# Kernel optimization log

Measured on AMD Instinct MI355X. Metric: run time of the kernel, lower is better.

The kernel has to match this reference:

```python
import jax, jax.numpy as jnp
import numpy as np

NI = 50000      # input nodes
NO = 50000      # output nodes
DEG = 16        # uniform neighborhood size -> E = NO*DEG
E = NO * DEG
FI = 64         # input feature dim
UNITS = 64
D = 3           # coord feature dim


def setup_inputs() -> dict:
    key = jax.random.key(0)
    k1, k2, k3, k4 = jax.random.split(key, 4)
    node_features = jax.random.normal(k1, (NI, FI), dtype=jnp.float32)
    coord_features = jax.random.normal(k2, (E, D), dtype=jnp.float32)
    indices = jax.random.randint(k3, (E,), 0, NI, dtype=jnp.int64)
    # uniform ragged structure: each output node has DEG edges
    row_splits = (jnp.arange(NO + 1, dtype=jnp.int64) * DEG)
    W = jax.random.normal(k4, (FI, UNITS * D), dtype=jnp.float32) * (1.0 / np.sqrt(FI))
    b = jnp.zeros((UNITS * D,), dtype=jnp.float32)
    return {"node_features": node_features, "coord_features": coord_features,
            "indices": indices, "row_splits": row_splits, "W": W, "b": b}


def reference(node_features, coord_features, indices, row_splits, W, b):
    # Dense projection on input nodes: [Ni, units*D]
    h = node_features @ W + b
    # gather_first=False path of ragged_convolution_transpose: gather after dense
    g = h[indices]                       # [E, units*D]
    g = g.reshape(-1, UNITS, D)          # [E, units, D]
    # contract over coord dim: f_eu = sum_d g_eud * coord_ed
    f = jnp.einsum('eud,ed->eu', g, coord_features)  # [E, units]
    # activation is None (identity)
    # ragged segment-sum via row_splits -> segment ids per edge
    num_out = row_splits.shape[0] - 1
    row_lengths = jnp.diff(row_splits)
    seg_ids = jnp.repeat(jnp.arange(num_out), row_lengths,
                         total_repeat_length=f.shape[0])
    out = jax.ops.segment_sum(f, seg_ids, num_segments=num_out)  # [No, units]
    return out
```

## Files before the change

### kernel.cpp

```cpp
#include <hip/hip_runtime.h>


#define NO 50000
#define DEG 16
#define FI 64
#define UNITS 64
#define KK 192
#define TN 16
#define NSTEP 6
#define GPAD 200
#define NBLK 1024
#define NTILES (NO / TN)

typedef __attribute__((ext_vector_type(8))) short short8;
typedef __attribute__((ext_vector_type(4))) float float4v;

static __device__ __forceinline__ unsigned int asu(float x){ union{float f;unsigned int u;}c; c.f=x; return c.u; }
static __device__ __forceinline__ float asf(unsigned int x){ union{unsigned int u;float f;}c; c.u=x; return c.f; }

__global__ __launch_bounds__(256, 4)
void rct3(const float* __restrict__ nf, const float* __restrict__ coord,
          const int* __restrict__ idx, const float* __restrict__ W,
          const float* __restrict__ b, float* __restrict__ out)
{
    __shared__ __align__(16) unsigned short Ghi[2][TN][GPAD];
    __shared__ __align__(16) unsigned short Glo[2][TN][GPAD];
    __shared__ float Cs[2][TN][4];

    const int tid  = threadIdx.x;
    const int w    = tid >> 6;
    const int lane = tid & 63;
    const int m16  = lane & 15;
    const int quad = lane >> 4;

    const int u = 16 * w + m16;
    short8 Bhi[NSTEP], Blo[NSTEP];
    #pragma unroll
    for (int s = 0; s < NSTEP; ++s) {
        #pragma unroll
        for (int j = 0; j < 8; ++j) {
            const int k = s * 32 + quad * 8 + j;
            const int i = k / 3, d = k - 3 * i;
            const float v = W[i * KK + 3 * u + d];
            const unsigned int vb = asu(v);
            const unsigned int rh = (vb + 0x7FFFu + ((vb >> 16) & 1u)) >> 16;
            const float hf = asf(rh << 16);
            Bhi[s][j] = (short)rh;
            Blo[s][j] = (short)(asu(v - hf) >> 16);
        }
    }
    const float b0 = b[3*u+0], b1 = b[3*u+1], b2 = b[3*u+2];

    int pp = 0;
    for (int t = blockIdx.x; t < NTILES; t += NBLK, pp ^= 1) {
        const int node0 = t * TN;

        #pragma unroll
        for (int r = 0; r < 4; ++r) {
            const int n  = 4 * w + r;
            const int eb = (node0 + n) * DEG;
            float a0=0.f,a1=0.f,a2=0.f,c0s=0.f,c1s=0.f,c2s=0.f;
            #pragma unroll
            for (int j = 0; j < DEG; ++j) {
                const int e  = __builtin_amdgcn_readfirstlane(eb + j);
                const int id = __builtin_amdgcn_readfirstlane(idx[e]);
                const float c0 = coord[3*e+0];
                const float c1 = coord[3*e+1];
                const float c2 = coord[3*e+2];
                const float v  = nf[id * FI + lane];
                a0 += v*c0; a1 += v*c1; a2 += v*c2;
                c0s += c0; c1s += c1; c2s += c2;
            }
            const unsigned int x0=asu(a0), x1=asu(a1), x2=asu(a2);
            Ghi[pp][n][3*lane+0] = (unsigned short)(x0>>16);
            Ghi[pp][n][3*lane+1] = (unsigned short)(x1>>16);
            Ghi[pp][n][3*lane+2] = (unsigned short)(x2>>16);
            Glo[pp][n][3*lane+0] = (unsigned short)(asu(a0 - asf(x0 & 0xFFFF0000u))>>16);
            Glo[pp][n][3*lane+1] = (unsigned short)(asu(a1 - asf(x1 & 0xFFFF0000u))>>16);
            Glo[pp][n][3*lane+2] = (unsigned short)(asu(a2 - asf(x2 & 0xFFFF0000u))>>16);
            if (lane == 0) {
                Cs[pp][n][0]=c0s; Cs[pp][n][1]=c1s; Cs[pp][n][2]=c2s; Cs[pp][n][3]=0.f;
            }
        }
        __syncthreads();

        float4v acc = {0.f, 0.f, 0.f, 0.f};
        #pragma unroll
        for (int s = 0; s < NSTEP; ++s) {
            const short8 Ahi = *(const short8*)(&Ghi[pp][m16][s*32 + quad*8]);
            const short8 Alo = *(const short8*)(&Glo[pp][m16][s*32 + quad*8]);
            acc = __builtin_amdgcn_mfma_f32_16x16x32_bf16(Ahi, Bhi[s], acc, 0, 0, 0);
            acc = __builtin_amdgcn_mfma_f32_16x16x32_bf16(Ahi, Blo[s], acc, 0, 0, 0);
            acc = __builtin_amdgcn_mfma_f32_16x16x32_bf16(Alo, Bhi[s], acc, 0, 0, 0);
        }

        #pragma unroll
        for (int reg = 0; reg < 4; ++reg) {
            const int row = quad * 4 + reg;
            const float4v c = *(const float4v*)(&Cs[pp][row][0]);
            out[(node0 + row) * UNITS + u] =
                acc[reg] + c[0]*b0 + c[1]*b1 + c[2]*b2;
        }
    }
}

extern "C" void kernel_launch(void* const* d_in, const int* in_sizes, int n_in,
                              void* d_out, int out_size, void* d_ws, size_t ws_size,
                              hipStream_t stream) {
    const float* nf    = (const float*)d_in[0];
    const float* coord = (const float*)d_in[1];
    const int*   idx   = (const int*)d_in[2];
    const float* W     = (const float*)d_in[4];
    const float* b     = (const float*)d_in[5];
    float* out = (float*)d_out;

    rct3<<<dim3(NBLK), dim3(256), 0, stream>>>(nf, coord, idx, W, b, out);
}
```

Before: 111.0 us.

## Prefetch edge indices and coords per-lane, broadcast via readlane, raise occupancy

Each wave now loads its 64 edge indices and coordinates in one coalesced per-lane load instead of scalar/broadcast loads per edge, then broadcasts them with readlane inside the gather loop. Metadata for the next tile is prefetched during the current tile, and the coordinate sums are computed by a shuffle reduction. The grid size and launch-bounds occupancy hint are also raised. This targets the latency of the serialized scalar index loads, at the cost of extra registers and readlane instructions.

```diff
diff --git a/kernel.cpp b/kernel.cpp
--- a/kernel.cpp
+++ b/kernel.cpp
@@ -9,7 +9,7 @@
 #define TN 16
 #define NSTEP 6
 #define GPAD 200
-#define NBLK 1024
+#define NBLK 1536
 #define NTILES (NO / TN)
 
 typedef __attribute__((ext_vector_type(8))) short short8;
@@ -17,15 +17,18 @@
 
 static __device__ __forceinline__ unsigned int asu(float x){ union{float f;unsigned int u;}c; c.f=x; return c.u; }
 static __device__ __forceinline__ float asf(unsigned int x){ union{unsigned int u;float f;}c; c.u=x; return c.f; }
+static __device__ __forceinline__ float rdlane_f(float v, int l){
+    return asf((unsigned int)__builtin_amdgcn_readlane((int)asu(v), l));
+}
 
-__global__ __launch_bounds__(256, 4)
+__global__ __launch_bounds__(256, 6)
 void rct3(const float* __restrict__ nf, const float* __restrict__ coord,
           const int* __restrict__ idx, const float* __restrict__ W,
           const float* __restrict__ b, float* __restrict__ out)
 {
     __shared__ __align__(16) unsigned short Ghi[2][TN][GPAD];
     __shared__ __align__(16) unsigned short Glo[2][TN][GPAD];
-    __shared__ float Cs[2][TN][4];
+    __shared__ __align__(16) float Cs[2][TN][4];
 
     const int tid  = threadIdx.x;
     const int w    = tid >> 6;
@@ -51,36 +54,67 @@
     }
     const float b0 = b[3*u+0], b1 = b[3*u+1], b2 = b[3*u+2];
 
+    int t = blockIdx.x;
+    int   vid;
+    float cv0, cv1, cv2;
+    {
+        const int e = (t * TN + 4 * w) * DEG + lane;
+        vid = idx[e];
+        cv0 = coord[3*e+0];
+        cv1 = coord[3*e+1];
+        cv2 = coord[3*e+2];
+    }
+
     int pp = 0;
-    for (int t = blockIdx.x; t < NTILES; t += NBLK, pp ^= 1) {
+    for (; t < NTILES; t += NBLK, pp ^= 1) {
         const int node0 = t * TN;
+
+        const int t2 = t + NBLK;
+        int   vidN = 0;
+        float cv0N = 0.f, cv1N = 0.f, cv2N = 0.f;
+        if (t2 < NTILES) {
+            const int e2 = (t2 * TN + 4 * w) * DEG + lane;
+            vidN = idx[e2];
+            cv0N = coord[3*e2+0];
+            cv1N = coord[3*e2+1];
+            cv2N = coord[3*e2+2];
+        }
+
+        {
+            float s0 = cv0, s1 = cv1, s2 = cv2;
+            #pragma unroll
+            for (int m = 1; m <= 8; m <<= 1) {
+                s0 += __shfl_xor(s0, m, 64);
+                s1 += __shfl_xor(s1, m, 64);
+                s2 += __shfl_xor(s2, m, 64);
+            }
+            if ((lane & 15) == 0) {
+                float4v cc = {s0, s1, s2, 0.f};
+                *(float4v*)(&Cs[pp][4*w + (lane >> 4)][0]) = cc;
+            }
+        }
 
         #pragma unroll
         for (int r = 0; r < 4; ++r) {
-            const int n  = 4 * w + r;
-            const int eb = (node0 + n) * DEG;
-            float a0=0.f,a1=0.f,a2=0.f,c0s=0.f,c1s=0.f,c2s=0.f;
+            const int n = 4 * w + r;
+            float a0 = 0.f, a1 = 0.f, a2 = 0.f;
             #pragma unroll
             for (int j = 0; j < DEG; ++j) {
-                const int e  = __builtin_amdgcn_readfirstlane(eb + j);
-                const int id = __builtin_amdgcn_readfirstlane(idx[e]);
-                const float c0 = coord[3*e+0];
-                const float c1 = coord[3*e+1];
-                const float c2 = coord[3*e+2];
+                const int l  = 16 * r + j;
+                const int id = __builtin_amdgcn_readlane(vid, l);
+                const float c0 = rdlane_f(cv0, l);
+                const float c1 = rdlane_f(cv1, l);
+                const float c2 = rdlane_f(cv2, l);
                 const float v  = nf[id * FI + lane];
-                a0 += v*c0; a1 += v*c1; a2 += v*c2;
-                c0s += c0; c1s += c1; c2s += c2;
+                a0 += v * c0; a1 += v * c1; a2 += v * c2;
             }
-            const unsigned int x0=asu(a0), x1=asu(a1), x2=asu(a2);
-            Ghi[pp][n][3*lane+0] = (unsigned short)(x0>>16);
-            Ghi[pp][n][3*lane+1] = (unsigned short)(x1>>16);
-            Ghi[pp][n][3*lane+2] = (unsigned short)(x2>>16);
-            Glo[pp][n][3*lane+0] = (unsigned short)(asu(a0 - asf(x0 & 0xFFFF0000u))>>16);
-            Glo[pp][n][3*lane+1] = (unsigned short)(asu(a1 - asf(x1 & 0xFFFF0000u))>>16);
-            Glo[pp][n][3*lane+2] = (unsigned short)(asu(a2 - asf(x2 & 0xFFFF0000u))>>16);
-            if (lane == 0) {
-                Cs[pp][n][0]=c0s; Cs[pp][n][1]=c1s; Cs[pp][n][2]=c2s; Cs[pp][n][3]=0.f;
-            }
+            const unsigned int x0 = asu(a0), x1 = asu(a1), x2 = asu(a2);
+            Ghi[pp][n][3*lane+0] = (unsigned short)(x0 >> 16);
+            Ghi[pp][n][3*lane+1] = (unsigned short)(x1 >> 16);
+            Ghi[pp][n][3*lane+2] = (unsigned short)(x2 >> 16);
+            Glo[pp][n][3*lane+0] = (unsigned short)(asu(a0 - asf(x0 & 0xFFFF0000u)) >> 16);
+            Glo[pp][n][3*lane+1] = (unsigned short)(asu(a1 - asf(x1 & 0xFFFF0000u)) >> 16);
+            Glo[pp][n][3*lane+2] = (unsigned short)(asu(a2 - asf(x2 & 0xFFFF0000u)) >> 16);
         }
         __syncthreads();
 
@@ -101,6 +135,8 @@
             out[(node0 + row) * UNITS + u] =
                 acc[reg] + c[0]*b0 + c[1]*b1 + c[2]*b2;
         }
+
+        vid = vidN; cv0 = cv0N; cv1 = cv1N; cv2 = cv2N;
     }
 }
 
```

Result: slower. 142.6 us (+28.5%).
